# Optimization experiments

Hardware: AMD Instinct MI355X
Metric: run time of the kernel (lower is better)

## Reference

```python
import jax, jax.numpy as jnp
import numpy as np

N = 100000
E = 1600000
IN_CH = 165
H1 = 128
H2 = 64
OUT = 2


def gcn_conv(x, W, b, src, dst, n):
    # PyG GCNConv: linear transform, add self-loops, symmetric normalization,
    # scatter-add aggregation, then bias.
    h = x @ W  # [n, out_ch]
    ones = jnp.ones(src.shape[0], dtype=h.dtype)
    deg = jax.ops.segment_sum(ones, dst, num_segments=n) + 1.0  # +1 for self-loop
    dinv = jax.lax.rsqrt(deg)
    norm = dinv[src] * dinv[dst]  # [E]
    agg = jax.ops.segment_sum(h[src] * norm[:, None], dst, num_segments=n)
    agg = agg + (dinv * dinv)[:, None] * h  # self-loop contribution
    return agg + b


def setup_inputs() -> dict:
    key = jax.random.key(0)
    ks = jax.random.split(key, 8)
    x = jax.random.normal(ks[0], (N, IN_CH), dtype=jnp.float32)
    edge_index = jax.random.randint(ks[1], (2, E), 0, N, dtype=jnp.int32)
    W1 = jax.random.normal(ks[2], (IN_CH, H1), dtype=jnp.float32) * (1.0 / np.sqrt(IN_CH))
    b1 = jnp.zeros((H1,), dtype=jnp.float32)
    W2 = jax.random.normal(ks[3], (H1, H2), dtype=jnp.float32) * (1.0 / np.sqrt(H1))
    b2 = jnp.zeros((H2,), dtype=jnp.float32)
    Wo = jax.random.normal(ks[4], (H2, OUT), dtype=jnp.float32) * (1.0 / np.sqrt(H2))
    bo = jnp.zeros((OUT,), dtype=jnp.float32)
    return {"x": x, "edge_index": edge_index, "W1": W1, "b1": b1,
            "W2": W2, "b2": b2, "Wo": Wo, "bo": bo}


def reference(x, edge_index, W1, b1, W2, b2, Wo, bo):
    src, dst = edge_index[0], edge_index[1]
    n = x.shape[0]
    h = jax.nn.relu(gcn_conv(x, W1, b1, src, dst, n))
    h = jax.nn.relu(gcn_conv(h, W2, b2, src, dst, n))
    return h @ Wo + bo  # [N, 2] logits
```

## Files before the change

### kernel.cpp

```cpp
#include <hip/hip_runtime.h>
#include <hip/hip_fp16.h>

#define N_NODES 100000
#define N_EDGES 1600000
#define IN_CH 165
#define H1C 128
#define H2C 64
#define K1PAD 192
#define CAP 64
#define SCATTER_BLOCKS 2048
#define PART_SZ 12500
#define GEMM1_BLOCKS ((N_NODES + 63) / 64)

typedef _Float16 half8 __attribute__((ext_vector_type(8)));
typedef float floatx4 __attribute__((ext_vector_type(4)));

__global__ __launch_bounds__(256) void prep(const float* __restrict__ W1,
                                            const float* __restrict__ W2,
                                            int* __restrict__ cnt,
                                            _Float16* __restrict__ w1t,
                                            _Float16* __restrict__ w2t) {
    int i = blockIdx.x * 256 + threadIdx.x;
    if (i < N_NODES) cnt[i] = 0;
    if (i < H1C * K1PAD) {
        int c = i / K1PAD, k = i - c * K1PAD;
        w1t[i] = (k < IN_CH) ? (_Float16)W1[k * H1C + c] : (_Float16)0.0f;
    }
    if (i < H2C * H1C) {
        int c = i >> 7, k = i & 127;
        w2t[i] = (_Float16)W2[k * H2C + c];
    }
}

__global__ void dinv_from_cnt(const int* __restrict__ cnt, float* __restrict__ dinv) {
    int i = blockIdx.x * 256 + threadIdx.x;
    if (i < N_NODES) dinv[i] = rsqrtf((float)cnt[i] + 1.0f);
}

__global__ __launch_bounds__(256) void scatter_and_gemm1(
        const int* __restrict__ ei, int* __restrict__ cnt, int* __restrict__ csr,
        const float* __restrict__ x, const _Float16* __restrict__ w1t,
        _Float16* __restrict__ h1) {
    __shared__ _Float16 lsA[64 * 200];
    int tid = threadIdx.x;

    if (blockIdx.x < SCATTER_BLOCKS) {
        int g  = blockIdx.x & 7;
        int bg = blockIdx.x >> 3;
        int lo = g * PART_SZ;
        int hi = lo + PART_SZ;
        const int* dstp = ei + N_EDGES;
        for (int e = bg * 256 + tid; e < N_EDGES; e += (SCATTER_BLOCKS / 8) * 256) {
            int d = __builtin_nontemporal_load(&dstp[e]);
            if (d >= lo && d < hi) {
                int s = __builtin_nontemporal_load(&ei[e]);
                int pos = atomicAdd(&cnt[d], 1);
                if (pos < CAP) csr[(d << 6) + pos] = s;
            }
        }
        return;
    }

    int bid = blockIdx.x - SCATTER_BLOCKS;
    int row0 = bid * 64;

    const int TILE_EL = 64 * IN_CH;
    int base = row0 * IN_CH;
    for (int idx = tid; idx < TILE_EL; idx += 256) {
        int r = idx / IN_CH;
        int k = idx - r * IN_CH;
        int g = base + idx;
        float v = (g < N_NODES * IN_CH) ? __builtin_nontemporal_load(&x[g]) : 0.0f;
        lsA[r * 200 + k] = (_Float16)v;
    }
    for (int idx = tid; idx < 64 * 35; idx += 256) {
        int r = idx / 35;
        int k = IN_CH + (idx - r * 35);
        lsA[r * 200 + k] = (_Float16)0.0f;
    }
    __syncthreads();

    int lane = tid & 63;
    int w = tid >> 6;
    int m = lane & 15;
    int q = lane >> 4;

    floatx4 acc[4][2] = {};
#pragma unroll
    for (int ks = 0; ks < 6; ++ks) {
        half8 af[4];
#pragma unroll
        for (int mt = 0; mt < 4; ++mt)
            af[mt] = *(const half8*)&lsA[(mt * 16 + m) * 200 + ks * 32 + q * 8];
        half8 bf[2];
#pragma unroll
        for (int nt = 0; nt < 2; ++nt)
            bf[nt] = *(const half8*)&w1t[((w * 2 + nt) * 16 + m) * K1PAD + ks * 32 + q * 8];
#pragma unroll
        for (int mt = 0; mt < 4; ++mt)
#pragma unroll
            for (int nt = 0; nt < 2; ++nt)
                acc[mt][nt] = __builtin_amdgcn_mfma_f32_16x16x32_f16(af[mt], bf[nt], acc[mt][nt], 0, 0, 0);
    }

#pragma unroll
    for (int mt = 0; mt < 4; ++mt) {
#pragma unroll
        for (int nt = 0; nt < 2; ++nt) {
            int col = (w * 2 + nt) * 16 + m;
#pragma unroll
            for (int reg = 0; reg < 4; ++reg) {
                int row = row0 + mt * 16 + q * 4 + reg;
                if (row < N_NODES)
                    __builtin_nontemporal_store((_Float16)acc[mt][nt][reg],
                                                &h1[(size_t)row * H1C + col]);
            }
        }
    }
}

__global__ __launch_bounds__(256) void agg1_gemm2(const __half* __restrict__ h,
                                                  const float* __restrict__ dinv,
                                                  const int* __restrict__ cnt,
                                                  const int* __restrict__ csr,
                                                  const float* __restrict__ b,
                                                  const _Float16* __restrict__ w2t,
                                                  _Float16* __restrict__ h2) {
    __shared__ _Float16 lsA[64 * 136];
    const __half2* hp = (const __half2*)h;
    int tid = threadIdx.x;
    int wave = tid >> 6;
    int lane = tid & 63;
    int row0 = blockIdx.x * 64;

    for (int i = 0; i < 16; ++i) {
        int r = wave * 16 + i;
        int node = row0 + r;
        if (node >= N_NODES) break;
        int deg = min(cnt[node], CAP);
        const int* cp = csr + ((size_t)node << 6);
        float di = dinv[node];
        float ax = 0.0f, ay = 0.0f;
        int e = 0;
        for (; e + 3 < deg; e += 4) {
            int s0 = cp[e], s1 = cp[e + 1], s2 = cp[e + 2], s3 = cp[e + 3];
            float n0 = dinv[s0], n1 = dinv[s1], n2 = dinv[s2], n3 = dinv[s3];
            float2 v0 = __half22float2(hp[(size_t)s0 * 64 + lane]);
            float2 v1 = __half22float2(hp[(size_t)s1 * 64 + lane]);
            float2 v2 = __half22float2(hp[(size_t)s2 * 64 + lane]);
            float2 v3 = __half22float2(hp[(size_t)s3 * 64 + lane]);
            ax += v0.x * n0 + v1.x * n1 + v2.x * n2 + v3.x * n3;
            ay += v0.y * n0 + v1.y * n1 + v2.y * n2 + v3.y * n3;
        }
        for (; e < deg; ++e) {
            int s0 = cp[e];
            float n0 = dinv[s0];
            float2 v0 = __half22float2(hp[(size_t)s0 * 64 + lane]);
            ax += v0.x * n0;
            ay += v0.y * n0;
        }
        float2 hv = __half22float2(hp[(size_t)node * 64 + lane]);
        float2 bv = *(const float2*)&b[lane * 2];
        float ox = fmaxf(ax * di + di * di * hv.x + bv.x, 0.0f);
        float oy = fmaxf(ay * di + di * di * hv.y + bv.y, 0.0f);
        *(__half2*)&lsA[r * 136 + lane * 2] = __floats2half2_rn(ox, oy);
    }
    __syncthreads();

    int w = tid >> 6;
    int m = lane & 15;
    int q = lane >> 4;

    floatx4 acc[4] = {};
#pragma unroll
    for (int ks = 0; ks < 4; ++ks) {
        half8 bf = *(const half8*)&w2t[(w * 16 + m) * H1C + ks * 32 + q * 8];
#pragma unroll
        for (int mt = 0; mt < 4; ++mt) {
            half8 af = *(const half8*)&lsA[(mt * 16 + m) * 136 + ks * 32 + q * 8];
            acc[mt] = __builtin_amdgcn_mfma_f32_16x16x32_f16(af, bf, acc[mt], 0, 0, 0);
        }
    }

    int col = w * 16 + m;
#pragma unroll
    for (int mt = 0; mt < 4; ++mt) {
#pragma unroll
        for (int reg = 0; reg < 4; ++reg) {
            int row = row0 + mt * 16 + q * 4 + reg;
            if (row < N_NODES) h2[(size_t)row * H2C + col] = (_Float16)acc[mt][reg];
        }
    }
}

__global__ __launch_bounds__(256) void agg_gather_64_final(const __half* __restrict__ h,
                                                           const float* __restrict__ dinv,
                                                           const int* __restrict__ cnt,
                                                           const int* __restrict__ csr,
                                                           const float* __restrict__ b,
                                                           const float* __restrict__ Wo,
                                                           const float* __restrict__ bo,
                                                           float* __restrict__ out) {
    int wave = threadIdx.x >> 6;
    int lane = threadIdx.x & 63;
    int node = blockIdx.x * 4 + wave;
    if (node >= N_NODES) return;
    int deg = min(cnt[node], CAP);
    const int* cp = csr + ((size_t)node << 6);
    float di = dinv[node];
    float acc = 0.0f;
    int e = 0;
    for (; e + 3 < deg; e += 4) {
        int s0 = cp[e], s1 = cp[e + 1], s2 = cp[e + 2], s3 = cp[e + 3];
        float n0 = dinv[s0], n1 = dinv[s1], n2 = dinv[s2], n3 = dinv[s3];
        float v0 = __half2float(h[(size_t)s0 * H2C + lane]);
        float v1 = __half2float(h[(size_t)s1 * H2C + lane]);
        float v2 = __half2float(h[(size_t)s2 * H2C + lane]);
        float v3 = __half2float(h[(size_t)s3 * H2C + lane]);
        acc += v0 * n0 + v1 * n1 + v2 * n2 + v3 * n3;
    }
    for (; e < deg; ++e) {
        int s0 = cp[e];
        acc += __half2float(h[(size_t)s0 * H2C + lane]) * dinv[s0];
    }
    float hv = __half2float(h[(size_t)node * H2C + lane]);
    float v = fmaxf(acc * di + di * di * hv + b[lane], 0.0f);
    float a0 = v * Wo[lane * 2];
    float a1 = v * Wo[lane * 2 + 1];
#pragma unroll
    for (int off = 32; off > 0; off >>= 1) {
        a0 += __shfl_down(a0, off, 64);
        a1 += __shfl_down(a1, off, 64);
    }
    if (lane == 0) {
        *(float2*)&out[(size_t)node * 2] = make_float2(a0 + bo[0], a1 + bo[1]);
    }
}

static inline char* align256(char* p) {
    return (char*)(((uintptr_t)p + 255) & ~(uintptr_t)255);
}

extern "C" void kernel_launch(void* const* d_in, const int* in_sizes, int n_in,
                              void* d_out, int out_size, void* d_ws, size_t ws_size,
                              hipStream_t stream) {
    const float* x  = (const float*)d_in[0];
    const int*   ei = (const int*)d_in[1];
    const float* W1 = (const float*)d_in[2];
    const float* b1 = (const float*)d_in[3];
    const float* W2 = (const float*)d_in[4];
    const float* b2 = (const float*)d_in[5];
    const float* Wo = (const float*)d_in[6];
    const float* bo = (const float*)d_in[7];
    float* out = (float*)d_out;

    char* wp = (char*)d_ws;
    int* cnt      = (int*)wp;        wp = align256(wp + sizeof(int) * N_NODES);
    int* csr      = (int*)wp;        wp = align256(wp + sizeof(int) * (size_t)N_NODES * CAP);
    float* dinv   = (float*)wp;      wp = align256(wp + sizeof(float) * N_NODES);
    _Float16* w1t = (_Float16*)wp;   wp = align256(wp + sizeof(_Float16) * H1C * K1PAD);
    _Float16* w2t = (_Float16*)wp;   wp = align256(wp + sizeof(_Float16) * H2C * H1C);
    _Float16* h1h = (_Float16*)wp;   wp = align256(wp + sizeof(_Float16) * (size_t)N_NODES * H1C);
    _Float16* h2h = (_Float16*)wp;   wp = align256(wp + sizeof(_Float16) * (size_t)N_NODES * H2C);

    const int nb_n   = (N_NODES + 255) / 256;
    const int nb_nd4 = (N_NODES + 3) / 4;

    prep<<<nb_n, 256, 0, stream>>>(W1, W2, cnt, w1t, w2t);

    scatter_and_gemm1<<<SCATTER_BLOCKS + GEMM1_BLOCKS, 256, 0, stream>>>(
        ei, cnt, csr, x, w1t, h1h);

    dinv_from_cnt<<<nb_n, 256, 0, stream>>>(cnt, dinv);

    agg1_gemm2<<<GEMM1_BLOCKS, 256, 0, stream>>>((const __half*)h1h, dinv, cnt, csr, b1,
                                                 w2t, h2h);

    agg_gather_64_final<<<nb_nd4, 256, 0, stream>>>((const __half*)h2h, dinv, cnt, csr,
                                                    b2, Wo, bo, out);
}
```

Measured before the change: 404.1 us.

## Slice feature matrices into 16-column planes for cache-friendly sliced aggregation

Stores h1 and h2 as column-sliced planes of 16 halves per node, and runs the aggregations per slice, 8 nodes per wave, with blockIdx interleaving slices so each slice's gather working set is smaller and more cache-resident. The fused agg1+gemm2 is split into a separate aggregation kernel writing a1 and a standalone MFMA gemm2. The final layer writes per-slice partial logits that a new reduce kernel sums. The scatter also loads edges as int4 vectors. This adds an extra round trip through global memory for a1, plus two more kernel launches.

Result: slower. 476.6 us (+18.0%).

```diff
diff --git a/kernel.cpp b/kernel.cpp
--- a/kernel.cpp
+++ b/kernel.cpp
@@ -11,9 +11,11 @@
 #define SCATTER_BLOCKS 2048
 #define PART_SZ 12500
 #define GEMM1_BLOCKS ((N_NODES + 63) / 64)
+#define NB128 ((N_NODES + 127) / 128)
 
 typedef _Float16 half8 __attribute__((ext_vector_type(8)));
 typedef float floatx4 __attribute__((ext_vector_type(4)));
+typedef int intx4 __attribute__((ext_vector_type(4)));
 
 __global__ __launch_bounds__(256) void prep(const float* __restrict__ W1,
                                             const float* __restrict__ W2,
@@ -49,13 +51,21 @@
         int bg = blockIdx.x >> 3;
         int lo = g * PART_SZ;
         int hi = lo + PART_SZ;
-        const int* dstp = ei + N_EDGES;
-        for (int e = bg * 256 + tid; e < N_EDGES; e += (SCATTER_BLOCKS / 8) * 256) {
-            int d = __builtin_nontemporal_load(&dstp[e]);
-            if (d >= lo && d < hi) {
-                int s = __builtin_nontemporal_load(&ei[e]);
-                int pos = atomicAdd(&cnt[d], 1);
-                if (pos < CAP) csr[(d << 6) + pos] = s;
+        const intx4* dst4 = (const intx4*)(ei + N_EDGES);
+        const intx4* src4 = (const intx4*)ei;
+        const int nchunks = N_EDGES / 4;
+        for (int i = bg * 256 + tid; i < nchunks; i += (SCATTER_BLOCKS / 8) * 256) {
+            intx4 d = __builtin_nontemporal_load(&dst4[i]);
+            bool m0 = (d.x >= lo) & (d.x < hi);
+            bool m1 = (d.y >= lo) & (d.y < hi);
+            bool m2 = (d.z >= lo) & (d.z < hi);
+            bool m3 = (d.w >= lo) & (d.w < hi);
+            if (m0 | m1 | m2 | m3) {
+                intx4 s = __builtin_nontemporal_load(&src4[i]);
+                if (m0) { int p = atomicAdd(&cnt[d.x], 1); if (p < CAP) csr[(d.x << 6) + p] = s.x; }
+                if (m1) { int p = atomicAdd(&cnt[d.y], 1); if (p < CAP) csr[(d.y << 6) + p] = s.y; }
+                if (m2) { int p = atomicAdd(&cnt[d.z], 1); if (p < CAP) csr[(d.z << 6) + p] = s.z; }
+                if (m3) { int p = atomicAdd(&cnt[d.w], 1); if (p < CAP) csr[(d.w << 6) + p] = s.w; }
             }
         }
         return;
@@ -107,134 +117,183 @@
     for (int mt = 0; mt < 4; ++mt) {
 #pragma unroll
         for (int nt = 0; nt < 2; ++nt) {
-            int col = (w * 2 + nt) * 16 + m;
+            _Float16* hs = h1 + (size_t)(w * 2 + nt) * N_NODES * 16;
 #pragma unroll
             for (int reg = 0; reg < 4; ++reg) {
                 int row = row0 + mt * 16 + q * 4 + reg;
-                if (row < N_NODES)
-                    __builtin_nontemporal_store((_Float16)acc[mt][nt][reg],
-                                                &h1[(size_t)row * H1C + col]);
+                if (row < N_NODES) hs[(size_t)row * 16 + m] = (_Float16)acc[mt][nt][reg];
             }
         }
     }
 }
 
-__global__ __launch_bounds__(256) void agg1_gemm2(const __half* __restrict__ h,
-                                                  const float* __restrict__ dinv,
-                                                  const int* __restrict__ cnt,
-                                                  const int* __restrict__ csr,
-                                                  const float* __restrict__ b,
+__global__ __launch_bounds__(256) void agg1_sliced(const _Float16* __restrict__ h1,
+                                                   const float* __restrict__ dinv,
+                                                   const int* __restrict__ cnt,
+                                                   const int* __restrict__ csr,
+                                                   const float* __restrict__ b,
+                                                   _Float16* __restrict__ a1) {
+    int g  = blockIdx.x & 7;
+    int nb = blockIdx.x >> 3;
+    int tid = threadIdx.x;
+    int wave = tid >> 6;
+    int lane = tid & 63;
+    int sub = lane >> 3;
+    int cl  = lane & 7;
+    const __half2* hg = (const __half2*)(h1 + (size_t)g * N_NODES * 16);
+    __half2* ag = (__half2*)(a1 + (size_t)g * N_NODES * 16);
+    const float2* b2p = (const float2*)b;
+
+#pragma unroll
+    for (int rep = 0; rep < 4; ++rep) {
+        int node = nb * 128 + rep * 32 + wave * 8 + sub;
+        if (node >= N_NODES) break;
+        int deg = min(cnt[node], CAP);
+        const int* cp = csr + ((size_t)node << 6);
+        const intx4* cp4 = (const intx4*)cp;
+        float ax = 0.0f, ay = 0.0f;
+        int e = 0;
+        for (; e + 3 < deg; e += 4) {
+            intx4 s = cp4[e >> 2];
+            float n0 = dinv[s.x], n1 = dinv[s.y], n2 = dinv[s.z], n3 = dinv[s.w];
+            float2 v0 = __half22float2(hg[(size_t)s.x * 8 + cl]);
+            float2 v1 = __half22float2(hg[(size_t)s.y * 8 + cl]);
+            float2 v2 = __half22float2(hg[(size_t)s.z * 8 + cl]);
+            float2 v3 = __half22float2(hg[(size_t)s.w * 8 + cl]);
+            ax += v0.x * n0 + v1.x * n1 + v2.x * n2 + v3.x * n3;
+            ay += v0.y * n0 + v1.y * n1 + v2.y * n2 + v3.y * n3;
+        }
+        for (; e < deg; ++e) {
+            int s0 = cp[e];
+            float n0 = dinv[s0];
+            float2 v0 = __half22float2(hg[(size_t)s0 * 8 + cl]);
+            ax += v0.x * n0;
+            ay += v0.y * n0;
+        }
+        float di = dinv[node];
+        float2 hv = __half22float2(hg[(size_t)node * 8 + cl]);
+        float2 bv = b2p[g * 8 + cl];
+        float ox = fmaxf(ax * di + di * di * hv.x + bv.x, 0.0f);
+        float oy = fmaxf(ay * di + di * di * hv.y + bv.y, 0.0f);
+        ag[(size_t)node * 8 + cl] = __floats2half2_rn(ox, oy);
+    }
+}
+
+__global__ __launch_bounds__(256) void gemm2_mfma(const _Float16* __restrict__ A,
                                                   const _Float16* __restrict__ w2t,
                                                   _Float16* __restrict__ h2) {
     __shared__ _Float16 lsA[64 * 136];
-    const __half2* hp = (const __half2*)h;
+    int tid = threadIdx.x;
+    int row0 = blockIdx.x * 64;
+
+    const uint* a1u = (const uint*)A;
+    for (int it = tid; it < 4096; it += 256) {
+        int g = it >> 9;
+        int rem = it & 511;
+        int r = rem >> 3;
+        int cl = rem & 7;
+        int row = row0 + r;
+        uint v = (row < N_NODES) ? a1u[(size_t)g * N_NODES * 8 + (size_t)row * 8 + cl] : 0u;
+        *(uint*)&lsA[r * 136 + (g * 8 + cl) * 2] = v;
+    }
+    __syncthreads();
+
+    int lane = tid & 63;
+    int w = tid >> 6;
+    int m = lane & 15;
+    int q = lane >> 4;
+
+    floatx4 acc[4] = {};
+#pragma unroll
+    for (int ks = 0; ks < 4; ++ks) {
+        half8 bf = *(const half8*)&w2t[(w * 16 + m) * H1C + ks * 32 + q * 8];
+#pragma unroll
+        for (int mt = 0; mt < 4; ++mt) {
+            half8 af = *(const half8*)&lsA[(mt * 16 + m) * 136 + ks * 32 + q * 8];
+            acc[mt] = __builtin_amdgcn_mfma_f32_16x16x32_f16(af, bf, acc[mt], 0, 0, 0);
+        }
+    }
+
+    _Float16* hs = h2 + (size_t)w * N_NODES * 16;
+#pragma unroll
+    for (int mt = 0; mt < 4; ++mt) {
+#pragma unroll
+        for (int reg = 0; reg < 4; ++reg) {
+            int row = row0 + mt * 16 + q * 4 + reg;
+            if (row < N_NODES) hs[(size_t)row * 16 + m] = (_Float16)acc[mt][reg];
+        }
+    }
+}
+
+__global__ __launch_bounds__(256) void agg2_sliced(const _Float16* __restrict__ h2,
+                                                   const float* __restrict__ dinv,
+                                                   const int* __restrict__ cnt,
+                                                   const int* __restrict__ csr,
+                                                   const float* __restrict__ b,
+                                                   const float* __restrict__ Wo,
+                                                   float2* __restrict__ part) {
+    int g  = blockIdx.x & 3;
+    int nb = blockIdx.x >> 2;
     int tid = threadIdx.x;
     int wave = tid >> 6;
     int lane = tid & 63;
-    int row0 = blockIdx.x * 64;
-
-    for (int i = 0; i < 16; ++i) {
-        int r = wave * 16 + i;
-        int node = row0 + r;
+    int sub = lane >> 3;
+    int cl  = lane & 7;
+    const __half2* hg = (const __half2*)(h2 + (size_t)g * N_NODES * 16);
+    int c0 = g * 16 + cl * 2;
+
+#pragma unroll
+    for (int rep = 0; rep < 4; ++rep) {
+        int node = nb * 128 + rep * 32 + wave * 8 + sub;
         if (node >= N_NODES) break;
         int deg = min(cnt[node], CAP);
         const int* cp = csr + ((size_t)node << 6);
-        float di = dinv[node];
+        const intx4* cp4 = (const intx4*)cp;
         float ax = 0.0f, ay = 0.0f;
         int e = 0;
         for (; e + 3 < deg; e += 4) {
-            int s0 = cp[e], s1 = cp[e + 1], s2 = cp[e + 2], s3 = cp[e + 3];
-            float n0 = dinv[s0], n1 = dinv[s1], n2 = dinv[s2], n3 = dinv[s3];
-            float2 v0 = __half22float2(hp[(size_t)s0 * 64 + lane]);
-            float2 v1 = __half22float2(hp[(size_t)s1 * 64 + lane]);
-            float2 v2 = __half22float2(hp[(size_t)s2 * 64 + lane]);
-            float2 v3 = __half22float2(hp[(size_t)s3 * 64 + lane]);
+            intx4 s = cp4[e >> 2];
+            float n0 = dinv[s.x], n1 = dinv[s.y], n2 = dinv[s.z], n3 = dinv[s.w];
+            float2 v0 = __half22float2(hg[(size_t)s.x * 8 + cl]);
+            float2 v1 = __half22float2(hg[(size_t)s.y * 8 + cl]);
+            float2 v2 = __half22float2(hg[(size_t)s.z * 8 + cl]);
+            float2 v3 = __half22float2(hg[(size_t)s.w * 8 + cl]);
             ax += v0.x * n0 + v1.x * n1 + v2.x * n2 + v3.x * n3;
             ay += v0.y * n0 + v1.y * n1 + v2.y * n2 + v3.y * n3;
         }
         for (; e < deg; ++e) {
             int s0 = cp[e];
             float n0 = dinv[s0];
-            float2 v0 = __half22float2(hp[(size_t)s0 * 64 + lane]);
+            float2 v0 = __half22float2(hg[(size_t)s0 * 8 + cl]);
             ax += v0.x * n0;
             ay += v0.y * n0;
         }
-        float2 hv = __half22float2(hp[(size_t)node * 64 + lane]);
-        float2 bv = *(const float2*)&b[lane * 2];
-        float ox = fmaxf(ax * di + di * di * hv.x + bv.x, 0.0f);
-        float oy = fmaxf(ay * di + di * di * hv.y + bv.y, 0.0f);
-        *(__half2*)&lsA[r * 136 + lane * 2] = __floats2half2_rn(ox, oy);
-    }
-    __syncthreads();
-
-    int w = tid >> 6;
-    int m = lane & 15;
-    int q = lane >> 4;
-
-    floatx4 acc[4] = {};
-#pragma unroll
-    for (int ks = 0; ks < 4; ++ks) {
-        half8 bf = *(const half8*)&w2t[(w * 16 + m) * H1C + ks * 32 + q * 8];
-#pragma unroll
-        for (int mt = 0; mt < 4; ++mt) {
-            half8 af = *(const half8*)&lsA[(mt * 16 + m) * 136 + ks * 32 + q * 8];
-            acc[mt] = __builtin_amdgcn_mfma_f32_16x16x32_f16(af, bf, acc[mt], 0, 0, 0);
-        }
-    }
-
-    int col = w * 16 + m;
-#pragma unroll
-    for (int mt = 0; mt < 4; ++mt) {
-#pragma unroll
-        for (int reg = 0; reg < 4; ++reg) {
-            int row = row0 + mt * 16 + q * 4 + reg;
-            if (row < N_NODES) h2[(size_t)row * H2C + col] = (_Float16)acc[mt][reg];
-        }
-    }
-}
-
-__global__ __launch_bounds__(256) void agg_gather_64_final(const __half* __restrict__ h,
-                                                           const float* __restrict__ dinv,
-                                                           const int* __restrict__ cnt,
-                                                           const int* __restrict__ csr,
-                                                           const float* __restrict__ b,
-                                                           const float* __restrict__ Wo,
-                                                           const float* __restrict__ bo,
-                                                           float* __restrict__ out) {
-    int wave = threadIdx.x >> 6;
-    int lane = threadIdx.x & 63;
-    int node = blockIdx.x * 4 + wave;
-    if (node >= N_NODES) return;
-    int deg = min(cnt[node], CAP);
-    const int* cp = csr + ((size_t)node << 6);
-    float di = dinv[node];
-    float acc = 0.0f;
-    int e = 0;
-    for (; e + 3 < deg; e += 4) {
-        int s0 = cp[e], s1 = cp[e + 1], s2 = cp[e + 2], s3 = cp[e + 3];
-        float n0 = dinv[s0], n1 = dinv[s1], n2 = dinv[s2], n3 = dinv[s3];
-        float v0 = __half2float(h[(size_t)s0 * H2C + lane]);
-        float v1 = __half2float(h[(size_t)s1 * H2C + lane]);
-        float v2 = __half2float(h[(size_t)s2 * H2C + lane]);
-        float v3 = __half2float(h[(size_t)s3 * H2C + lane]);
-        acc += v0 * n0 + v1 * n1 + v2 * n2 + v3 * n3;
-    }
-    for (; e < deg; ++e) {
-        int s0 = cp[e];
-        acc += __half2float(h[(size_t)s0 * H2C + lane]) * dinv[s0];
-    }
-    float hv = __half2float(h[(size_t)node * H2C + lane]);
-    float v = fmaxf(acc * di + di * di * hv + b[lane], 0.0f);
-    float a0 = v * Wo[lane * 2];
-    float a1 = v * Wo[lane * 2 + 1];
-#pragma unroll
-    for (int off = 32; off > 0; off >>= 1) {
-        a0 += __shfl_down(a0, off, 64);
-        a1 += __shfl_down(a1, off, 64);
-    }
-    if (lane == 0) {
-        *(float2*)&out[(size_t)node * 2] = make_float2(a0 + bo[0], a1 + bo[1]);
-    }
+        float di = dinv[node];
+        float2 hv = __half22float2(hg[(size_t)node * 8 + cl]);
+        float vx = fmaxf(ax * di + di * di * hv.x + b[c0], 0.0f);
+        float vy = fmaxf(ay * di + di * di * hv.y + b[c0 + 1], 0.0f);
+        float a0 = vx * Wo[c0 * 2] + vy * Wo[(c0 + 1) * 2];
+        float a1 = vx * Wo[c0 * 2 + 1] + vy * Wo[(c0 + 1) * 2 + 1];
+#pragma unroll
+        for (int off = 1; off < 8; off <<= 1) {
+            a0 += __shfl_xor(a0, off, 64);
+            a1 += __shfl_xor(a1, off, 64);
+        }
+        if (cl == 0) part[(size_t)g * N_NODES + node] = make_float2(a0, a1);
+    }
+}
+
+__global__ void final_reduce(const float2* __restrict__ part, const float* __restrict__ bo,
+                             float* __restrict__ out) {
+    int i = blockIdx.x * 256 + threadIdx.x;
+    if (i >= N_NODES) return;
+    float2 p0 = part[i];
+    float2 p1 = part[(size_t)N_NODES + i];
+    float2 p2 = part[(size_t)2 * N_NODES + i];
+    float2 p3 = part[(size_t)3 * N_NODES + i];
+    float2 o = make_float2(p0.x + p1.x + p2.x + p3.x + bo[0],
+                           p0.y + p1.y + p2.y + p3.y + bo[1]);
+    *(float2*)&out[(size_t)i * 2] = o;
 }
 
 static inline char* align256(char* p) {
@@ -261,10 +320,11 @@
     _Float16* w1t = (_Float16*)wp;   wp = align256(wp + sizeof(_Float16) * H1C * K1PAD);
     _Float16* w2t = (_Float16*)wp;   wp = align256(wp + sizeof(_Float16) * H2C * H1C);
     _Float16* h1h = (_Float16*)wp;   wp = align256(wp + sizeof(_Float16) * (size_t)N_NODES * H1C);
+    _Float16* a1h = (_Float16*)wp;   wp = align256(wp + sizeof(_Float16) * (size_t)N_NODES * H1C);
     _Float16* h2h = (_Float16*)wp;   wp = align256(wp + sizeof(_Float16) * (size_t)N_NODES * H2C);
-
-    const int nb_n   = (N_NODES + 255) / 256;
-    const int nb_nd4 = (N_NODES + 3) / 4;
+    float2* part  = (float2*)wp;     wp = align256(wp + sizeof(float2) * (size_t)4 * N_NODES);
+
+    const int nb_n = (N_NODES + 255) / 256;
 
     prep<<<nb_n, 256, 0, stream>>>(W1, W2, cnt, w1t, w2t);
 
@@ -273,9 +333,11 @@
 
     dinv_from_cnt<<<nb_n, 256, 0, stream>>>(cnt, dinv);
 
-    agg1_gemm2<<<GEMM1_BLOCKS, 256, 0, stream>>>((const __half*)h1h, dinv, cnt, csr, b1,
-                                                 w2t, h2h);
-
-    agg_gather_64_final<<<nb_nd4, 256, 0, stream>>>((const __half*)h2h, dinv, cnt, csr,
-                                                    b2, Wo, bo, out);
-}
+    agg1_sliced<<<NB128 * 8, 256, 0, stream>>>(h1h, dinv, cnt, csr, b1, a1h);
+
+    gemm2_mfma<<<(N_NODES + 63) / 64, 256, 0, stream>>>(a1h, w2t, h2h);
+
+    agg2_sliced<<<NB128 * 4, 256, 0, stream>>>(h2h, dinv, cnt, csr, b2, Wo, part);
+
+    final_reduce<<<nb_n, 256, 0, stream>>>(part, bo, out);
+}
```
